# Optimization experiments

Measured on AMD Instinct MI355X. Metric: run time of the kernel, lower is better.

The kernel has to match this reference:

```python
import jax, jax.numpy as jnp
import numpy as np
import math

B, S, DIM, HEADS, HEAD_DIM = 2, 2048, 1024, 16, 64
ROT_DIM, ROPE_THETA = 64, 10000.0


def make_rope(seq_len):
    # DitRotary.forward: theta over half rotary_dim, duplicated interleaved pairs
    theta = 1.0 / (ROPE_THETA ** (np.arange(0, ROT_DIM, 2, dtype=np.float32) / ROT_DIM))
    pos = np.arange(seq_len, dtype=np.float32).reshape(-1, 1)
    idx = pos * theta  # [S, 32]
    cos = np.stack((np.cos(idx), np.cos(idx)), axis=-1).reshape(seq_len, -1)  # [S, 64]
    sin = np.stack((np.sin(idx), np.sin(idx)), axis=-1).reshape(seq_len, -1)
    # unsqueeze(2).unsqueeze(1) -> [1, S, 1, 64]
    return jnp.asarray(cos)[None, :, None, :], jnp.asarray(sin)[None, :, None, :]


def rotate_half(x):
    # interleaved-pair rotation: (x1, x2) -> (-x2, x1)
    x = x.reshape(*x.shape[:-1], -1, 2)
    x1, x2 = x[..., 0], x[..., 1]
    return jnp.stack((-x2, x1), axis=-1).reshape(*x.shape[:-2], -1)


def apply_rotary(x, cos, sin):
    return x * cos + rotate_half(x) * sin


def setup_inputs() -> dict:
    key = jax.random.key(0)
    ks = jax.random.split(key, 8)
    sc = 1.0 / math.sqrt(DIM)
    x = jax.random.normal(ks[0], (B, S, DIM), dtype=jnp.float32)
    cos, sin = make_rope(S)
    Wq = jax.random.normal(ks[1], (DIM, DIM), dtype=jnp.float32) * sc
    bq = jnp.zeros((DIM,), jnp.float32)
    Wk = jax.random.normal(ks[2], (DIM, DIM), dtype=jnp.float32) * sc
    bk = jnp.zeros((DIM,), jnp.float32)
    Wv = jax.random.normal(ks[3], (DIM, DIM), dtype=jnp.float32) * sc
    bv = jnp.zeros((DIM,), jnp.float32)
    Wo = jax.random.normal(ks[4], (DIM, DIM), dtype=jnp.float32) * sc
    bo = jnp.zeros((DIM,), jnp.float32)
    mask = jnp.ones((B, 1, 1, S), dtype=bool)
    return {"x": x, "cos": cos, "sin": sin, "Wq": Wq, "bq": bq, "Wk": Wk,
            "bk": bk, "Wv": Wv, "bv": bv, "Wo": Wo, "bo": bo, "mask": mask}


def reference(x, cos, sin, Wq, bq, Wk, bk, Wv, bv, Wo, bo, mask):
    b, s, _ = x.shape
    q = (x @ Wq.T + bq).reshape(b, s, HEADS, HEAD_DIM)
    k = (x @ Wk.T + bk).reshape(b, s, HEADS, HEAD_DIM)
    v = (x @ Wv.T + bv).reshape(b, s, HEADS, HEAD_DIM)
    # partial rotary: applied only to head index 0 (dim 2 of [B,S,H,D])
    q = jnp.concatenate([apply_rotary(q[:, :, :1, :], cos, sin), q[:, :, 1:, :]], axis=2)
    k = jnp.concatenate([apply_rotary(k[:, :, :1, :], cos, sin), k[:, :, 1:, :]], axis=2)
    # [B,H,S,D]
    q = q.transpose(0, 2, 1, 3)
    k = k.transpose(0, 2, 1, 3)
    v = v.transpose(0, 2, 1, 3)
    neg = jnp.finfo(jnp.float32).min
    attn_mask = jnp.where(mask, 0.0, neg)  # ~mask * finfo.min
    scores = jnp.einsum("bhsd,bhtd->bhst", q, k) / math.sqrt(HEAD_DIM)
    scores = scores + attn_mask
    probs = jax.nn.softmax(scores.astype(jnp.float32), axis=-1).astype(q.dtype)
    out = jnp.einsum("bhst,bhtd->bhsd", probs, v)
    out = out.transpose(0, 2, 1, 3).reshape(b, s, HEADS * HEAD_DIM)
    return out @ Wo.T + bo
```

## Files before the change

kernel.cpp:

```cpp
#include <hip/hip_runtime.h>
#include <hip/hip_bf16.h>


typedef __attribute__((ext_vector_type(8))) __bf16 bf16x8;
typedef __attribute__((ext_vector_type(4))) __bf16 bf16x4;
typedef __attribute__((ext_vector_type(4))) float f32x4;
typedef __attribute__((ext_vector_type(4))) short s16x4;

#define NB_B 2
#define NB_S 2048
#define NB_DIM 1024
#define NB_H 16
#define NB_HD 64
#define NB_BS (NB_B * NB_S)

__device__ __forceinline__ void async_cp16(const __bf16* g, __bf16* l) {
    __builtin_amdgcn_global_load_lds(
        (const __attribute__((address_space(1))) unsigned int*)g,
        (__attribute__((address_space(3))) unsigned int*)l, 16, 0, 0);
}

__global__ __launch_bounds__(256) void cvt_kernel(
    const float* __restrict__ x,  const float* __restrict__ wq,
    const float* __restrict__ wk, const float* __restrict__ wv,
    const float* __restrict__ wo,
    __bf16* __restrict__ xb,  __bf16* __restrict__ wqb,
    __bf16* __restrict__ wkb, __bf16* __restrict__ wvb,
    __bf16* __restrict__ wob) {
    const int XQ = (NB_BS * NB_DIM) / 4;
    const int WQ = (NB_DIM * NB_DIM) / 4;
    int i = blockIdx.x * 256 + threadIdx.x;
    const float* src; __bf16* dst; int off;
    if (i < XQ)              { src = x;  dst = xb;  off = i; }
    else if (i < XQ + WQ)    { src = wq; dst = wqb; off = i - XQ; }
    else if (i < XQ + 2*WQ)  { src = wk; dst = wkb; off = i - XQ - WQ; }
    else if (i < XQ + 3*WQ)  { src = wv; dst = wvb; off = i - XQ - 2*WQ; }
    else                     { src = wo; dst = wob; off = i - XQ - 3*WQ; }
    f32x4 v = *(const f32x4*)(src + (size_t)off * 4);
    bf16x4 b;
#pragma unroll
    for (int j = 0; j < 4; ++j) b[j] = (__bf16)v[j];
    *(bf16x4*)(dst + (size_t)off * 4) = b;
}

__global__ __launch_bounds__(256) void gemm_qkv_kernel(
    const __bf16* __restrict__ A,
    const float* __restrict__ cosb, const float* __restrict__ sinb,
    const __bf16* __restrict__ Wq, const float* __restrict__ bq, __bf16* __restrict__ qbuf,
    const __bf16* __restrict__ Wk, const float* __restrict__ bk, __bf16* __restrict__ kbuf,
    const __bf16* __restrict__ Wv, const float* __restrict__ bv, __bf16* __restrict__ vtbuf) {
    constexpr int K = 1024;
    __shared__ __align__(16) __bf16 As[128][64];
    __shared__ __align__(16) __bf16 Bs[128][64];

    const int z = blockIdx.z;
    const __bf16* W; const float* bias;
    if (z == 0)      { W = Wq; bias = bq; }
    else if (z == 1) { W = Wk; bias = bk; }
    else             { W = Wv; bias = bv; }

    const int tid = threadIdx.x;
    const int lane = tid & 63;
    const int w = tid >> 6;
    const int wm = w >> 1, wn = w & 1;
    const int row16 = lane & 15, quad = lane >> 4;
    const int r7 = row16 & 7;
    const int m0 = blockIdx.x * 128, n0 = blockIdx.y * 128;

    f32x4 acc[4][4] = {};

    for (int kt = 0; kt < K; kt += 64) {
        __syncthreads();
#pragma unroll
        for (int i = 0; i < 4; ++i) {
            int c = tid + i * 256;
            int row = c >> 3, g = c & 7;
            int gcol = (g ^ (row & 7)) << 3;
            async_cp16(A + (size_t)(m0 + row) * K + kt + gcol, &As[row][g << 3]);
            async_cp16(W + (size_t)(n0 + row) * K + kt + gcol, &Bs[row][g << 3]);
        }
        __syncthreads();

        bf16x8 af[4][2], bfr[4][2];
#pragma unroll
        for (int t = 0; t < 4; ++t)
#pragma unroll
            for (int kk = 0; kk < 2; ++kk) {
                af[t][kk]  = *(const bf16x8*)&As[wm * 64 + t * 16 + row16][((kk * 4 + quad) ^ r7) << 3];
                bfr[t][kk] = *(const bf16x8*)&Bs[wn * 64 + t * 16 + row16][((kk * 4 + quad) ^ r7) << 3];
            }
        __builtin_amdgcn_s_setprio(1);
#pragma unroll
        for (int mt = 0; mt < 4; ++mt)
#pragma unroll
            for (int nt = 0; nt < 4; ++nt)
#pragma unroll
                for (int kk = 0; kk < 2; ++kk)
                    acc[mt][nt] = __builtin_amdgcn_mfma_f32_16x16x32_bf16(af[mt][kk], bfr[nt][kk], acc[mt][nt], 0, 0, 0);
        __builtin_amdgcn_s_setprio(0);
    }

    if (z == 2) {
#pragma unroll
        for (int mt = 0; mt < 4; ++mt) {
            int row = m0 + wm * 64 + mt * 16 + quad * 4;
            int b = row >> 11, s = row & (NB_S - 1);
#pragma unroll
            for (int nt = 0; nt < 4; ++nt) {
                int col = n0 + wn * 64 + nt * 16 + row16;
                float bv = bias[col];
                bf16x4 pack;
#pragma unroll
                for (int r = 0; r < 4; ++r) pack[r] = (__bf16)(acc[mt][nt][r] + bv);
                *(bf16x4*)&vtbuf[(size_t)b * (NB_DIM * NB_S) + (size_t)col * NB_S + s] = pack;
            }
        }
    } else {
        __bf16* C = (z == 0) ? qbuf : kbuf;
        const bool rope = (n0 == 0) && (wn == 0);
#pragma unroll
        for (int mt = 0; mt < 4; ++mt) {
            int row = m0 + wm * 64 + mt * 16 + quad * 4;
#pragma unroll
            for (int nt = 0; nt < 4; ++nt) {
                int col = n0 + wn * 64 + nt * 16 + row16;
                float bv = bias[col];
#pragma unroll
                for (int r = 0; r < 4; ++r) {
                    float val = acc[mt][nt][r] + bv;
                    if (rope) {
                        float part = __shfl_xor(val, 1, 64);
                        int srow = (row + r) & (NB_S - 1);
                        float c  = cosb[srow * 64 + col];
                        float sn = sinb[srow * 64 + col];
                        val = (lane & 1) ? (val * c + part * sn) : (val * c - part * sn);
                    }
                    C[(size_t)(row + r) * NB_DIM + col] = (__bf16)val;
                }
            }
        }
    }
}

__global__ __launch_bounds__(256) void gemm_o_kernel(
    const __bf16* __restrict__ A, const __bf16* __restrict__ W,
    const float* __restrict__ bias, float* __restrict__ C) {
    constexpr int K = 1024;
    constexpr int NT = K / 32;
    __shared__ __align__(16) __bf16 As[3][128][32];
    __shared__ __align__(16) __bf16 Bs[3][64][32];

    const int tid = threadIdx.x;
    const int lane = tid & 63;
    const int w = tid >> 6;
    const int row16 = lane & 15, quad = lane >> 4;
    const int m0 = blockIdx.x * 128, n0 = blockIdx.y * 64;

    f32x4 acc[2][4] = {};

    auto stage = [&](int nb, int kt) {
#pragma unroll
        for (int i = 0; i < 2; ++i) {
            int c = tid + i * 256;
            int row = c >> 2;
            int co = (c & 3) << 3;
            async_cp16(A + (size_t)(m0 + row) * K + kt + co, &As[nb][row][co]);
        }
        {
            int row = tid >> 2;
            int co = (tid & 3) << 3;
            async_cp16(W + (size_t)(n0 + row) * K + kt + co, &Bs[nb][row][co]);
        }
    };
    auto compute = [&](int nb) {
        bf16x8 af[2], bfr[4];
#pragma unroll
        for (int t = 0; t < 2; ++t)
            af[t] = *(const bf16x8*)&As[nb][w * 32 + t * 16 + row16][quad * 8];
#pragma unroll
        for (int nt = 0; nt < 4; ++nt)
            bfr[nt] = *(const bf16x8*)&Bs[nb][nt * 16 + row16][quad * 8];
        __builtin_amdgcn_s_setprio(1);
#pragma unroll
        for (int mt = 0; mt < 2; ++mt)
#pragma unroll
            for (int nt = 0; nt < 4; ++nt)
                acc[mt][nt] = __builtin_amdgcn_mfma_f32_16x16x32_bf16(af[mt], bfr[nt], acc[mt][nt], 0, 0, 0);
        __builtin_amdgcn_s_setprio(0);
    };

    stage(0, 0);
    stage(1, 32);
    int cu = 0, pfb = 2;
    for (int t = 0; t < NT - 1; ++t) {
        asm volatile("s_waitcnt vmcnt(3)" ::: "memory");
        __builtin_amdgcn_s_barrier();
        if (t + 2 < NT) stage(pfb, (t + 2) * 32);
        compute(cu);
        cu  = (cu  == 2) ? 0 : cu + 1;
        pfb = (pfb == 2) ? 0 : pfb + 1;
    }
    asm volatile("s_waitcnt vmcnt(0)" ::: "memory");
    __builtin_amdgcn_s_barrier();
    compute(cu);

#pragma unroll
    for (int mt = 0; mt < 2; ++mt) {
        int row = m0 + w * 32 + mt * 16 + quad * 4;
#pragma unroll
        for (int nt = 0; nt < 4; ++nt) {
            int col = n0 + nt * 16 + row16;
            float bv = bias[col];
#pragma unroll
            for (int r = 0; r < 4; ++r)
                C[(size_t)(row + r) * NB_DIM + col] = acc[mt][nt][r] + bv;
        }
    }
}

__global__ __launch_bounds__(512) void attn_kernel(const __bf16* __restrict__ qb,
                                                   const __bf16* __restrict__ kb,
                                                   const __bf16* __restrict__ vtb,
                                                   __bf16* __restrict__ ob) {
    __shared__ __align__(16) __bf16 Ks[128][72];
    __shared__ __align__(16) __bf16 Vts[64][132];

    const int tid = threadIdx.x;
    const int lane = tid & 63;
    const int w = tid >> 6;
    const int row16 = lane & 15, quad = lane >> 4;
    const int bh = blockIdx.y;
    const int b = bh >> 4, h = bh & 15;
    const int q0 = blockIdx.x * 256 + w * 32;

    const size_t headoff = (size_t)b * NB_S * NB_DIM + (size_t)h * NB_HD;
    const size_t vtoff = (size_t)b * (NB_DIM * NB_S) + (size_t)(h * NB_HD) * NB_S;

    const float qscale = 0.18033688011112042f;
    bf16x8 qf[2][2];
#pragma unroll
    for (int m = 0; m < 2; ++m)
#pragma unroll
        for (int hh = 0; hh < 2; ++hh) {
            bf16x8 v = *(const bf16x8*)(qb + headoff + (size_t)(q0 + m * 16 + row16) * NB_DIM + hh * 32 + quad * 8);
#pragma unroll
            for (int j = 0; j < 8; ++j) v[j] = (__bf16)((float)v[j] * qscale);
            qf[m][hh] = v;
        }

    f32x4 o[2][4] = {};
    f32x4 ol[2] = {};

    const short one_bf16 = (short)0x3F80;
    const s16x4 onesf = {one_bf16, one_bf16, one_bf16, one_bf16};

    bf16x8 kreg[2], vreg[2];
#pragma unroll
    for (int i = 0; i < 2; ++i) {
        int c = tid + i * 512;
        kreg[i] = *(const bf16x8*)(kb + headoff + (size_t)(c >> 3) * NB_DIM + ((c & 7) << 3));
        vreg[i] = *(const bf16x8*)(vtb + vtoff + (size_t)(c >> 4) * NB_S + ((c & 15) << 3));
    }

    for (int kt = 0; kt < 16; ++kt) {
        __syncthreads();
#pragma unroll
        for (int i = 0; i < 2; ++i) {
            int c = tid + i * 512;
            *(bf16x8*)&Ks[c >> 3][(c & 7) << 3] = kreg[i];
            bf16x4 lo, hi;
#pragma unroll
            for (int j = 0; j < 4; ++j) { lo[j] = vreg[i][j]; hi[j] = vreg[i][j + 4]; }
            *(bf16x4*)&Vts[c >> 4][(c & 15) << 3] = lo;
            *(bf16x4*)&Vts[c >> 4][((c & 15) << 3) + 4] = hi;
        }
        __syncthreads();
        if (kt < 15) {
            int base = (kt + 1) * 128;
#pragma unroll
            for (int i = 0; i < 2; ++i) {
                int c = tid + i * 512;
                kreg[i] = *(const bf16x8*)(kb + headoff + (size_t)(base + (c >> 3)) * NB_DIM + ((c & 7) << 3));
                vreg[i] = *(const bf16x8*)(vtb + vtoff + (size_t)(c >> 4) * NB_S + base + ((c & 15) << 3));
            }
        }

        s16x4 pf[2][8];
#pragma unroll
        for (int t = 0; t < 8; ++t) {
            f32x4 s0 = {}, s1 = {};
            __builtin_amdgcn_s_setprio(1);
#pragma unroll
            for (int hh = 0; hh < 2; ++hh) {
                bf16x8 kf = *(const bf16x8*)&Ks[t * 16 + row16][hh * 32 + quad * 8];
                s0 = __builtin_amdgcn_mfma_f32_16x16x32_bf16(kf, qf[0][hh], s0, 0, 0, 0);
                s1 = __builtin_amdgcn_mfma_f32_16x16x32_bf16(kf, qf[1][hh], s1, 0, 0, 0);
            }
            __builtin_amdgcn_s_setprio(0);
            bf16x4 p0, p1;
#pragma unroll
            for (int r = 0; r < 4; ++r) {
                float e0 = __builtin_amdgcn_exp2f(s0[r]); p0[r] = (__bf16)e0;
                float e1 = __builtin_amdgcn_exp2f(s1[r]); p1[r] = (__bf16)e1;
            }
            pf[0][t] = __builtin_bit_cast(s16x4, p0);
            pf[1][t] = __builtin_bit_cast(s16x4, p1);
            ol[0] = __builtin_amdgcn_mfma_f32_16x16x16bf16_1k(pf[0][t], onesf, ol[0], 0, 0, 0);
            ol[1] = __builtin_amdgcn_mfma_f32_16x16x16bf16_1k(pf[1][t], onesf, ol[1], 0, 0, 0);
        }

        __builtin_amdgcn_s_setprio(1);
#pragma unroll
        for (int nt = 0; nt < 4; ++nt)
#pragma unroll
            for (int t = 0; t < 8; ++t) {
                s16x4 vf = *(const s16x4*)&Vts[nt * 16 + row16][t * 16 + quad * 4];
                o[0][nt] = __builtin_amdgcn_mfma_f32_16x16x16bf16_1k(pf[0][t], vf, o[0][nt], 0, 0, 0);
                o[1][nt] = __builtin_amdgcn_mfma_f32_16x16x16bf16_1k(pf[1][t], vf, o[1][nt], 0, 0, 0);
            }
        __builtin_amdgcn_s_setprio(0);
    }

#pragma unroll
    for (int m = 0; m < 2; ++m)
#pragma unroll
        for (int r = 0; r < 4; ++r) {
            float inv = 1.f / ol[m][r];
            int row = q0 + m * 16 + quad * 4 + r;
#pragma unroll
            for (int nt = 0; nt < 4; ++nt)
                ob[headoff + (size_t)row * NB_DIM + nt * 16 + row16] = (__bf16)(o[m][nt][r] * inv);
        }
}

extern "C" void kernel_launch(void* const* d_in, const int* in_sizes, int n_in,
                              void* d_out, int out_size, void* d_ws, size_t ws_size,
                              hipStream_t stream) {
    const float* x    = (const float*)d_in[0];
    const float* cosb = (const float*)d_in[1];
    const float* sinb = (const float*)d_in[2];
    const float* Wq   = (const float*)d_in[3];
    const float* bq   = (const float*)d_in[4];
    const float* Wk   = (const float*)d_in[5];
    const float* bk   = (const float*)d_in[6];
    const float* Wv   = (const float*)d_in[7];
    const float* bv   = (const float*)d_in[8];
    const float* Wo   = (const float*)d_in[9];
    const float* bo   = (const float*)d_in[10];

    __bf16* qbuf  = (__bf16*)d_ws;
    __bf16* kbuf  = qbuf + (size_t)NB_BS * NB_DIM;
    __bf16* vtbuf = kbuf + (size_t)NB_BS * NB_DIM;
    __bf16* abuf  = vtbuf + (size_t)NB_BS * NB_DIM;
    __bf16* xb    = abuf + (size_t)NB_BS * NB_DIM;
    __bf16* wqb   = xb + (size_t)NB_BS * NB_DIM;
    __bf16* wkb   = wqb + (size_t)NB_DIM * NB_DIM;
    __bf16* wvb   = wkb + (size_t)NB_DIM * NB_DIM;
    __bf16* wob   = wvb + (size_t)NB_DIM * NB_DIM;

    const int XQ = (NB_BS * NB_DIM) / 4, WQ = (NB_DIM * NB_DIM) / 4;
    cvt_kernel<<<(XQ + 4 * WQ) / 256, 256, 0, stream>>>(x, Wq, Wk, Wv, Wo,
                                                        xb, wqb, wkb, wvb, wob);

    dim3 gqkv(NB_BS / 128, NB_DIM / 128, 3);
    gemm_qkv_kernel<<<gqkv, 256, 0, stream>>>(xb, cosb, sinb,
                                              wqb, bq, qbuf,
                                              wkb, bk, kbuf,
                                              wvb, bv, vtbuf);

    attn_kernel<<<dim3(NB_S / 256, NB_B * NB_H), 512, 0, stream>>>(qbuf, kbuf, vtbuf, abuf);

    dim3 go(NB_BS / 128, NB_DIM / 64);
    gemm_o_kernel<<<go, 256, 0, stream>>>(abuf, wob, bo, (float*)d_out);
}
```

Measured before the change: 201.1 us.

## Rework O-projection GEMM staging and enlarge attention per-warp query tile

```diff
diff --git a/kernel.cpp b/kernel.cpp
--- a/kernel.cpp
+++ b/kernel.cpp
@@ -146,63 +146,57 @@
     const __bf16* __restrict__ A, const __bf16* __restrict__ W,
     const float* __restrict__ bias, float* __restrict__ C) {
     constexpr int K = 1024;
-    constexpr int NT = K / 32;
-    __shared__ __align__(16) __bf16 As[3][128][32];
-    __shared__ __align__(16) __bf16 Bs[3][64][32];
+    __shared__ __align__(16) __bf16 As[128][64];
+    __shared__ __align__(16) __bf16 Bs[64][64];
 
     const int tid = threadIdx.x;
     const int lane = tid & 63;
     const int w = tid >> 6;
     const int row16 = lane & 15, quad = lane >> 4;
+    const int r7 = row16 & 7;
     const int m0 = blockIdx.x * 128, n0 = blockIdx.y * 64;
 
     f32x4 acc[2][4] = {};
 
-    auto stage = [&](int nb, int kt) {
+    for (int kt = 0; kt < K; kt += 64) {
+        __syncthreads();
+#pragma unroll
+        for (int i = 0; i < 4; ++i) {
+            int c = tid + i * 256;
+            int row = c >> 3, g = c & 7;
+            int gcol = (g ^ (row & 7)) << 3;
+            async_cp16(A + (size_t)(m0 + row) * K + kt + gcol, &As[row][g << 3]);
+        }
 #pragma unroll
         for (int i = 0; i < 2; ++i) {
             int c = tid + i * 256;
-            int row = c >> 2;
-            int co = (c & 3) << 3;
-            async_cp16(A + (size_t)(m0 + row) * K + kt + co, &As[nb][row][co]);
-        }
-        {
-            int row = tid >> 2;
-            int co = (tid & 3) << 3;
-            async_cp16(W + (size_t)(n0 + row) * K + kt + co, &Bs[nb][row][co]);
-        }
-    };
-    auto compute = [&](int nb) {
-        bf16x8 af[2], bfr[4];
+            int row = c >> 3, g = c & 7;
+            int gcol = (g ^ (row & 7)) << 3;
+            async_cp16(W + (size_t)(n0 + row) * K + kt + gcol, &Bs[row][g << 3]);
+        }
+        __syncthreads();
+
+        bf16x8 af[2][2], bfr[4][2];
 #pragma unroll
         for (int t = 0; t < 2; ++t)
-            af[t] = *(const bf16x8*)&As[nb][w * 32 + t * 16 + row16][quad * 8];
+#pragma unroll
+            for (int kk = 0; kk < 2; ++kk)
+                af[t][kk] = *(const bf16x8*)&As[w * 32 + t * 16 + row16][((kk * 4 + quad) ^ r7) << 3];
 #pragma unroll
         for (int nt = 0; nt < 4; ++nt)
-            bfr[nt] = *(const bf16x8*)&Bs[nb][nt * 16 + row16][quad * 8];
+#pragma unroll
+            for (int kk = 0; kk < 2; ++kk)
+                bfr[nt][kk] = *(const bf16x8*)&Bs[nt * 16 + row16][((kk * 4 + quad) ^ r7) << 3];
         __builtin_amdgcn_s_setprio(1);
 #pragma unroll
         for (int mt = 0; mt < 2; ++mt)
 #pragma unroll
             for (int nt = 0; nt < 4; ++nt)
-                acc[mt][nt] = __builtin_amdgcn_mfma_f32_16x16x32_bf16(af[mt], bfr[nt], acc[mt][nt], 0, 0, 0);
+#pragma unroll
+                for (int kk = 0; kk < 2; ++kk)
+                    acc[mt][nt] = __builtin_amdgcn_mfma_f32_16x16x32_bf16(af[mt][kk], bfr[nt][kk], acc[mt][nt], 0, 0, 0);
         __builtin_amdgcn_s_setprio(0);
-    };
-
-    stage(0, 0);
-    stage(1, 32);
-    int cu = 0, pfb = 2;
-    for (int t = 0; t < NT - 1; ++t) {
-        asm volatile("s_waitcnt vmcnt(3)" ::: "memory");
-        __builtin_amdgcn_s_barrier();
-        if (t + 2 < NT) stage(pfb, (t + 2) * 32);
-        compute(cu);
-        cu  = (cu  == 2) ? 0 : cu + 1;
-        pfb = (pfb == 2) ? 0 : pfb + 1;
-    }
-    asm volatile("s_waitcnt vmcnt(0)" ::: "memory");
-    __builtin_amdgcn_s_barrier();
-    compute(cu);
+    }
 
 #pragma unroll
     for (int mt = 0; mt < 2; ++mt) {
@@ -218,7 +212,7 @@
     }
 }
 
-__global__ __launch_bounds__(512) void attn_kernel(const __bf16* __restrict__ qb,
+__global__ __launch_bounds__(256) void attn_kernel(const __bf16* __restrict__ qb,
                                                    const __bf16* __restrict__ kb,
                                                    const __bf16* __restrict__ vtb,
                                                    __bf16* __restrict__ ob) {
@@ -229,17 +223,17 @@
     const int lane = tid & 63;
     const int w = tid >> 6;
     const int row16 = lane & 15, quad = lane >> 4;
-    const int bh = blockIdx.y;
+    const int bh = blockIdx.x;
     const int b = bh >> 4, h = bh & 15;
-    const int q0 = blockIdx.x * 256 + w * 32;
+    const int q0 = blockIdx.y * 256 + w * 64;
 
     const size_t headoff = (size_t)b * NB_S * NB_DIM + (size_t)h * NB_HD;
     const size_t vtoff = (size_t)b * (NB_DIM * NB_S) + (size_t)(h * NB_HD) * NB_S;
 
     const float qscale = 0.18033688011112042f;
-    bf16x8 qf[2][2];
-#pragma unroll
-    for (int m = 0; m < 2; ++m)
+    bf16x8 qf[4][2];
+#pragma unroll
+    for (int m = 0; m < 4; ++m)
 #pragma unroll
         for (int hh = 0; hh < 2; ++hh) {
             bf16x8 v = *(const bf16x8*)(qb + headoff + (size_t)(q0 + m * 16 + row16) * NB_DIM + hh * 32 + quad * 8);
@@ -248,16 +242,16 @@
             qf[m][hh] = v;
         }
 
-    f32x4 o[2][4] = {};
-    f32x4 ol[2] = {};
+    f32x4 o[4][4] = {};
+    f32x4 ol[4] = {};
 
     const short one_bf16 = (short)0x3F80;
     const s16x4 onesf = {one_bf16, one_bf16, one_bf16, one_bf16};
 
-    bf16x8 kreg[2], vreg[2];
-#pragma unroll
-    for (int i = 0; i < 2; ++i) {
-        int c = tid + i * 512;
+    bf16x8 kreg[4], vreg[4];
+#pragma unroll
+    for (int i = 0; i < 4; ++i) {
+        int c = tid + i * 256;
         kreg[i] = *(const bf16x8*)(kb + headoff + (size_t)(c >> 3) * NB_DIM + ((c & 7) << 3));
         vreg[i] = *(const bf16x8*)(vtb + vtoff + (size_t)(c >> 4) * NB_S + ((c & 15) << 3));
     }
@@ -265,8 +259,8 @@
     for (int kt = 0; kt < 16; ++kt) {
         __syncthreads();
 #pragma unroll
-        for (int i = 0; i < 2; ++i) {
-            int c = tid + i * 512;
+        for (int i = 0; i < 4; ++i) {
+            int c = tid + i * 256;
             *(bf16x8*)&Ks[c >> 3][(c & 7) << 3] = kreg[i];
             bf16x4 lo, hi;
 #pragma unroll
@@ -278,51 +272,48 @@
         if (kt < 15) {
             int base = (kt + 1) * 128;
 #pragma unroll
-            for (int i = 0; i < 2; ++i) {
-                int c = tid + i * 512;
+            for (int i = 0; i < 4; ++i) {
+                int c = tid + i * 256;
                 kreg[i] = *(const bf16x8*)(kb + headoff + (size_t)(base + (c >> 3)) * NB_DIM + ((c & 7) << 3));
                 vreg[i] = *(const bf16x8*)(vtb + vtoff + (size_t)(c >> 4) * NB_S + base + ((c & 15) << 3));
             }
         }
 
-        s16x4 pf[2][8];
 #pragma unroll
         for (int t = 0; t < 8; ++t) {
-            f32x4 s0 = {}, s1 = {};
+            f32x4 s[4] = {};
             __builtin_amdgcn_s_setprio(1);
 #pragma unroll
             for (int hh = 0; hh < 2; ++hh) {
                 bf16x8 kf = *(const bf16x8*)&Ks[t * 16 + row16][hh * 32 + quad * 8];
-                s0 = __builtin_amdgcn_mfma_f32_16x16x32_bf16(kf, qf[0][hh], s0, 0, 0, 0);
-                s1 = __builtin_amdgcn_mfma_f32_16x16x32_bf16(kf, qf[1][hh], s1, 0, 0, 0);
+#pragma unroll
+                for (int m = 0; m < 4; ++m)
+                    s[m] = __builtin_amdgcn_mfma_f32_16x16x32_bf16(kf, qf[m][hh], s[m], 0, 0, 0);
             }
             __builtin_amdgcn_s_setprio(0);
-            bf16x4 p0, p1;
-#pragma unroll
-            for (int r = 0; r < 4; ++r) {
-                float e0 = __builtin_amdgcn_exp2f(s0[r]); p0[r] = (__bf16)e0;
-                float e1 = __builtin_amdgcn_exp2f(s1[r]); p1[r] = (__bf16)e1;
-            }
-            pf[0][t] = __builtin_bit_cast(s16x4, p0);
-            pf[1][t] = __builtin_bit_cast(s16x4, p1);
-            ol[0] = __builtin_amdgcn_mfma_f32_16x16x16bf16_1k(pf[0][t], onesf, ol[0], 0, 0, 0);
-            ol[1] = __builtin_amdgcn_mfma_f32_16x16x16bf16_1k(pf[1][t], onesf, ol[1], 0, 0, 0);
-        }
-
-        __builtin_amdgcn_s_setprio(1);
-#pragma unroll
-        for (int nt = 0; nt < 4; ++nt)
-#pragma unroll
-            for (int t = 0; t < 8; ++t) {
+            s16x4 pfm[4];
+#pragma unroll
+            for (int m = 0; m < 4; ++m) {
+                bf16x4 p;
+#pragma unroll
+                for (int r = 0; r < 4; ++r) p[r] = (__bf16)__builtin_amdgcn_exp2f(s[m][r]);
+                pfm[m] = __builtin_bit_cast(s16x4, p);
+                ol[m] = __builtin_amdgcn_mfma_f32_16x16x16bf16_1k(pfm[m], onesf, ol[m], 0, 0, 0);
+            }
+            __builtin_amdgcn_s_setprio(1);
+#pragma unroll
+            for (int nt = 0; nt < 4; ++nt) {
                 s16x4 vf = *(const s16x4*)&Vts[nt * 16 + row16][t * 16 + quad * 4];
-                o[0][nt] = __builtin_amdgcn_mfma_f32_16x16x16bf16_1k(pf[0][t], vf, o[0][nt], 0, 0, 0);
-                o[1][nt] = __builtin_amdgcn_mfma_f32_16x16x16bf16_1k(pf[1][t], vf, o[1][nt], 0, 0, 0);
-            }
-        __builtin_amdgcn_s_setprio(0);
-    }
-
-#pragma unroll
-    for (int m = 0; m < 2; ++m)
+#pragma unroll
+                for (int m = 0; m < 4; ++m)
+                    o[m][nt] = __builtin_amdgcn_mfma_f32_16x16x16bf16_1k(pfm[m], vf, o[m][nt], 0, 0, 0);
+            }
+            __builtin_amdgcn_s_setprio(0);
+        }
+    }
+
+#pragma unroll
+    for (int m = 0; m < 4; ++m)
 #pragma unroll
         for (int r = 0; r < 4; ++r) {
             float inv = 1.f / ol[m][r];
@@ -368,7 +359,7 @@
                                               wkb, bk, kbuf,
                                               wvb, bv, vtbuf);
 
-    attn_kernel<<<dim3(NB_S / 256, NB_B * NB_H), 512, 0, stream>>>(qbuf, kbuf, vtbuf, abuf);
+    attn_kernel<<<dim3(NB_B * NB_H, NB_S / 256), 256, 0, stream>>>(qbuf, kbuf, vtbuf, abuf);
 
     dim3 go(NB_BS / 128, NB_DIM / 64);
     gemm_o_kernel<<<go, 256, 0, stream>>>(abuf, wob, bo, (float*)d_out);
```

New measurement: 206.1 us. 2.5% more time.
